# Kernel tuning notes

Measured on AMD Instinct MI355X. Metric: run time of the kernel, lower is better.

The kernel has to match this reference:

```python
import jax, jax.numpy as jnp
import numpy as np

N = 50000   # nodes
E = 600000  # edges
D = 128     # in = hidden = out channels (must be equal per the cat/mean readout)
B = 4096    # number of lookup indices


def setup_inputs() -> dict:
    key = jax.random.key(0)
    ks = jax.random.split(key, 8)
    x = jax.random.normal(ks[0], (N, D), dtype=jnp.float32)
    edge_index = jax.random.randint(ks[1], (2, E), 0, N)
    edge_weight = jax.random.uniform(ks[2], (E,), dtype=jnp.float32)
    inputs_idx = jax.random.randint(ks[3], (B,), 0, N + 1)  # N is the appended zero row
    def lin_w(k, din, dout):
        return jax.random.normal(k, (din, dout), dtype=jnp.float32) / np.sqrt(din).astype(np.float32)
    W1 = lin_w(ks[4], D, D); b1 = jnp.zeros((D,), jnp.float32)
    W2 = lin_w(ks[5], D, D); b2 = jnp.zeros((D,), jnp.float32)
    W3 = lin_w(ks[6], D, D); b3 = jnp.zeros((D,), jnp.float32)
    return {"inputs_idx": inputs_idx, "x": x, "edge_index": edge_index,
            "edge_weight": edge_weight, "W1": W1, "b1": b1, "W2": W2,
            "b2": b2, "W3": W3, "b3": b3}


def gcn_conv(x, W, b, src, dst, w):
    # PyG GCNConv with add_self_loops=True (fill weight 1) and symmetric norm.
    deg = jnp.zeros((N,), x.dtype).at[dst].add(w) + 1.0  # self-loop contributes 1
    dinv = jax.lax.rsqrt(deg)
    norm = dinv[src] * w * dinv[dst]                      # [E]
    h = x @ W                                             # [N, D]
    agg = jax.ops.segment_sum(norm[:, None] * h[src], dst, num_segments=N)
    agg = agg + h * (dinv * dinv)[:, None]                # self-loop term: deg^-1 * h
    return agg + b


def lookup(x, inputs_idx):
    # append a zero row, then gather
    x_ = jnp.concatenate([x, jnp.zeros((1, x.shape[-1]), x.dtype)], axis=0)
    return x_[inputs_idx]  # [B, D]


def reference(inputs_idx, x, edge_index, edge_weight, W1, b1, W2, b2, W3, b3):
    src, dst = edge_index[0], edge_index[1]
    x1 = jax.nn.relu(gcn_conv(x, W1, b1, src, dst, edge_weight))
    x2 = jax.nn.relu(gcn_conv(x1, W2, b2, src, dst, edge_weight))
    x3 = jax.nn.relu(gcn_conv(x2, W3, b3, src, dst, edge_weight))
    e1 = lookup(x1, inputs_idx)
    e2 = lookup(x2, inputs_idx)
    e3 = lookup(x3, inputs_idx)
    # torch.cat([1,B,D]x3, dim=0).mean(0) == elementwise mean of the three
    return (e1 + e2 + e3) / 3.0
```

## Files before the change

kernel.cpp:

```cpp
#include <hip/hip_runtime.h>
#include <hip/hip_fp16.h>

#define D 128
#define STRIDE 48

typedef _Float16 f16x8 __attribute__((ext_vector_type(8)));
typedef float f32x4 __attribute__((ext_vector_type(4)));
struct h4 { __half2 a, b; };

__global__ __launch_bounds__(256) void build_kernel(
    const int* __restrict__ ei, const float* __restrict__ ew,
    unsigned long long* __restrict__ packed, int2* __restrict__ pairs, int E) {
  int e = blockIdx.x * 256 + threadIdx.x;
  if (e >= E) return;
  int s = ei[e], d = ei[E + e];
  float w = ew[e];
  unsigned long long add =
      (1ull << 40) | (unsigned long long)(unsigned int)__float2uint_rn(w * 16777216.0f);
  unsigned long long old = atomicAdd(&packed[d], add);
  int rank = (int)(old >> 40);
  if (rank < STRIDE) pairs[(size_t)d * STRIDE + rank] = make_int2(s, __float_as_int(w));
}

__global__ __launch_bounds__(256) void dinv_cnt_kernel(
    const unsigned long long* __restrict__ packed, float* __restrict__ dinv,
    int* __restrict__ cnt, int N) {
  int i = blockIdx.x * 256 + threadIdx.x;
  if (i >= N) return;
  unsigned long long p = packed[i];
  int c = (int)(p >> 40);
  cnt[i] = c < STRIDE ? c : STRIDE;
  float deg = (float)(p & ((1ull << 40) - 1)) * (1.0f / 16777216.0f) + 1.0f;
  dinv[i] = rsqrtf(deg);
}

__global__ __launch_bounds__(256) void tohalf_kernel(
    const float* __restrict__ in, __half* __restrict__ out, int n4) {
  int t = blockIdx.x * 256 + threadIdx.x;
  if (t >= n4) return;
  float4 v = ((const float4*)in)[t];
  h4 o = {__floats2half2_rn(v.x, v.y), __floats2half2_rn(v.z, v.w)};
  ((h4*)out)[t] = o;
}

__global__ __launch_bounds__(256) void wtrans_kernel(
    const float* __restrict__ W1, const float* __restrict__ W2,
    const float* __restrict__ W3, __half* __restrict__ WT1,
    __half* __restrict__ WT2, __half* __restrict__ WT3) {
  int t = blockIdx.x * 256 + threadIdx.x;
  if (t >= 3 * D * D) return;
  int m = t >> 14;
  int i = t & (D * D - 1);
  int k = i >> 7, n = i & 127;
  const float* W = (m == 0) ? W1 : (m == 1) ? W2 : W3;
  __half* WT = (m == 0) ? WT1 : (m == 1) ? WT2 : WT3;
  WT[n * D + k] = __float2half(W[k * D + n]);
}

__global__ __launch_bounds__(256) void agg_kernel(
    const __half* __restrict__ x16, const float* __restrict__ dinv,
    const int* __restrict__ cnt, const int2* __restrict__ pairs,
    __half* __restrict__ agg16, int N) {
  int gw = (blockIdx.x * 256 + threadIdx.x) >> 6;
  int lane = threadIdx.x & 63;
  if (gw >= N) return;
  float di = dinv[gw];
  int c = cnt[gw];
  const int2* pr = pairs + (size_t)gw * STRIDE;
  float2 acc = __half22float2(((const __half2*)(x16 + (size_t)gw * D))[lane]);
  acc.x *= di * di;
  acc.y *= di * di;
  int e = 0;
  for (; e + 4 <= c; e += 4) {
    int2 p0 = pr[e], p1 = pr[e + 1], p2 = pr[e + 2], p3 = pr[e + 3];
    float n0 = dinv[p0.x] * __int_as_float(p0.y) * di;
    float n1 = dinv[p1.x] * __int_as_float(p1.y) * di;
    float n2 = dinv[p2.x] * __int_as_float(p2.y) * di;
    float n3 = dinv[p3.x] * __int_as_float(p3.y) * di;
    float2 v0 = __half22float2(((const __half2*)(x16 + (size_t)p0.x * D))[lane]);
    float2 v1 = __half22float2(((const __half2*)(x16 + (size_t)p1.x * D))[lane]);
    float2 v2 = __half22float2(((const __half2*)(x16 + (size_t)p2.x * D))[lane]);
    float2 v3 = __half22float2(((const __half2*)(x16 + (size_t)p3.x * D))[lane]);
    acc.x += n0 * v0.x + n1 * v1.x + n2 * v2.x + n3 * v3.x;
    acc.y += n0 * v0.y + n1 * v1.y + n2 * v2.y + n3 * v3.y;
  }
  for (; e < c; e++) {
    int2 p0 = pr[e];
    float n0 = dinv[p0.x] * __int_as_float(p0.y) * di;
    float2 v0 = __half22float2(((const __half2*)(x16 + (size_t)p0.x * D))[lane]);
    acc.x += n0 * v0.x;
    acc.y += n0 * v0.y;
  }
  ((__half2*)(agg16 + (size_t)gw * D))[lane] = __floats2half2_rn(acc.x, acc.y);
}

__global__ __launch_bounds__(256) void gemm16(
    const __half* __restrict__ A16, const __half* __restrict__ WT,
    const float* __restrict__ bias, __half* __restrict__ out16, int n) {
  __shared__ __half Bs[D * D];
  const int tid = threadIdx.x;
  const int wid = tid >> 6;
  const int lane = tid & 63;
  const int l15 = lane & 15;
  const int lk = lane >> 4;
  const int rbase = blockIdx.x * 64 + wid * 16;

  f16x8 a[4];
  {
    int r = rbase + l15;
    bool ok = (r < n);
    const __half* arow = A16 + (size_t)r * D + lk * 8;
#pragma unroll
    for (int kk = 0; kk < 4; kk++) {
      f16x8 z = {0, 0, 0, 0, 0, 0, 0, 0};
      a[kk] = ok ? *(const f16x8*)(arow + kk * 32) : z;
    }
  }
  {
    const int4* src = (const int4*)WT;
#pragma unroll
    for (int i = 0; i < 8; i++) {
      int slot = tid + i * 256;
      int byte = slot << 4;
      int row = byte >> 8;
      int4 v = src[slot];
      *(int4*)((char*)Bs + (byte ^ ((row & 7) << 4))) = v;
    }
  }
  __syncthreads();

  f32x4 c[8];
#pragma unroll
  for (int nf = 0; nf < 8; nf++) c[nf] = (f32x4){0.f, 0.f, 0.f, 0.f};

#pragma unroll
  for (int kk = 0; kk < 4; kk++) {
#pragma unroll
    for (int nf = 0; nf < 8; nf++) {
      int byte = ((nf * 16 + l15) << 8) + (kk << 6) + (lk << 4);
      byte ^= (l15 & 7) << 4;
      f16x8 b = *(const f16x8*)((const char*)Bs + byte);
      c[nf] = __builtin_amdgcn_mfma_f32_16x16x32_f16(a[kk], b, c[nf], 0, 0, 0);
    }
  }

#pragma unroll
  for (int nf = 0; nf < 8; nf++) {
    float bv = bias[nf * 16 + l15];
    int r0 = rbase + lk * 4;
#pragma unroll
    for (int rg = 0; rg < 4; rg++) {
      int r = r0 + rg;
      if (r < n) {
        float v = fmaxf(c[nf][rg] + bv, 0.f);
        out16[(size_t)r * D + nf * 16 + l15] = __float2half(v);
      }
    }
  }
}

__global__ __launch_bounds__(256) void lookup_kernel(
    const __half* __restrict__ xl, const int* __restrict__ idx,
    float* __restrict__ out, int B, int N, int add) {
  int t = blockIdx.x * 256 + threadIdx.x;
  if (t >= B * 16) return;
  int b = t >> 4, c8 = t & 15;
  int id = idx[b];
  float4 o0 = make_float4(0.f, 0.f, 0.f, 0.f);
  float4 o1 = make_float4(0.f, 0.f, 0.f, 0.f);
  if ((unsigned)id < (unsigned)N) {
    int4 raw = *(const int4*)(xl + (size_t)id * D + c8 * 8);
    const __half2* h = (const __half2*)&raw;
    float2 f0 = __half22float2(h[0]);
    float2 f1 = __half22float2(h[1]);
    float2 f2 = __half22float2(h[2]);
    float2 f3 = __half22float2(h[3]);
    o0 = make_float4(f0.x, f0.y, f1.x, f1.y);
    o1 = make_float4(f2.x, f2.y, f3.x, f3.y);
  }
  const float s = 1.0f / 3.0f;
  float* op = out + (size_t)b * D + c8 * 8;
  if (add) {
    float4 p0 = *(float4*)op, p1 = *(float4*)(op + 4);
    p0.x += o0.x * s; p0.y += o0.y * s; p0.z += o0.z * s; p0.w += o0.w * s;
    p1.x += o1.x * s; p1.y += o1.y * s; p1.z += o1.z * s; p1.w += o1.w * s;
    *(float4*)op = p0; *(float4*)(op + 4) = p1;
  } else {
    float4 p0 = make_float4(o0.x * s, o0.y * s, o0.z * s, o0.w * s);
    float4 p1 = make_float4(o1.x * s, o1.y * s, o1.z * s, o1.w * s);
    *(float4*)op = p0; *(float4*)(op + 4) = p1;
  }
}


extern "C" void kernel_launch(void* const* d_in, const int* in_sizes, int n_in,
                              void* d_out, int out_size, void* d_ws, size_t ws_size,
                              hipStream_t stream) {
  const int*   inputs_idx  = (const int*)d_in[0];
  const float* x           = (const float*)d_in[1];
  const int*   edge_index  = (const int*)d_in[2];
  const float* edge_weight = (const float*)d_in[3];
  const float* W1 = (const float*)d_in[4];
  const float* b1 = (const float*)d_in[5];
  const float* W2 = (const float*)d_in[6];
  const float* b2 = (const float*)d_in[7];
  const float* W3 = (const float*)d_in[8];
  const float* b3 = (const float*)d_in[9];
  float* out = (float*)d_out;

  const int B = in_sizes[0];
  const int N = in_sizes[1] / D;
  const int E = in_sizes[3];
  (void)n_in; (void)out_size; (void)ws_size;

  char* p = (char*)d_ws;
  size_t off = 0;
  auto alloc = [&](size_t bytes) -> void* {
    void* r = p + off;
    off += (bytes + 255) & ~(size_t)255;
    return r;
  };
  unsigned long long* packed = (unsigned long long*)alloc((size_t)N * 8);
  float*  dinv  = (float*)alloc((size_t)N * 4);
  int*    cnt   = (int*)alloc((size_t)N * 4);
  int2*   pairs = (int2*)alloc((size_t)N * STRIDE * 8);
  __half* x16   = (__half*)alloc((size_t)N * D * 2);
  __half* aggT  = (__half*)alloc((size_t)N * D * 2);
  __half* oA    = (__half*)alloc((size_t)N * D * 2);
  __half* oB    = (__half*)alloc((size_t)N * D * 2);
  __half* WT1   = (__half*)alloc((size_t)D * D * 2);
  __half* WT2   = (__half*)alloc((size_t)D * D * 2);
  __half* WT3   = (__half*)alloc((size_t)D * D * 2);

  hipMemsetAsync(packed, 0, (size_t)N * 8, stream);

  int eb = (E + 255) / 256;
  build_kernel<<<eb, 256, 0, stream>>>(edge_index, edge_weight, packed, pairs, E);
  dinv_cnt_kernel<<<(N + 255) / 256, 256, 0, stream>>>(packed, dinv, cnt, N);
  int n4 = N * D / 4;
  tohalf_kernel<<<(n4 + 255) / 256, 256, 0, stream>>>(x, x16, n4);
  wtrans_kernel<<<(3 * D * D + 255) / 256, 256, 0, stream>>>(W1, W2, W3, WT1, WT2, WT3);

  int ab = (N + 3) / 4;
  int gb = (N + 63) / 64;
  int lb = (B * 16 + 255) / 256;

  agg_kernel<<<ab, 256, 0, stream>>>(x16, dinv, cnt, pairs, aggT, N);
  gemm16<<<gb, 256, 0, stream>>>(aggT, WT1, b1, oA, N);
  lookup_kernel<<<lb, 256, 0, stream>>>(oA, inputs_idx, out, B, N, 0);
  agg_kernel<<<ab, 256, 0, stream>>>(oA, dinv, cnt, pairs, aggT, N);
  gemm16<<<gb, 256, 0, stream>>>(aggT, WT2, b2, oB, N);
  lookup_kernel<<<lb, 256, 0, stream>>>(oB, inputs_idx, out, B, N, 1);
  agg_kernel<<<ab, 256, 0, stream>>>(oB, dinv, cnt, pairs, aggT, N);
  gemm16<<<gb, 256, 0, stream>>>(aggT, WT3, b3, oA, N);
  lookup_kernel<<<lb, 256, 0, stream>>>(oA, inputs_idx, out, B, N, 1);
}
```

Baseline: 193.2 us.

## Precompute per-edge GCN norms once and split aggregation across channel blocks

The 64-bit packed atomic (count plus fixed-point weight) becomes a plain int count atomic. Degree is now summed from the stored pair weights by a per-node wavefront reduction, and a new norm kernel rewrites each pair's weight in place as dinv[src]*w*dinv[dst]. The three aggregation passes therefore no longer gather dinv per edge. Aggregation also moves to a 2D grid where 16 lanes per node each cover a 32-channel slice across 4 y-blocks, trading fewer wasted lanes and more parallelism for re-reading the pair list four times per node.

```diff
diff --git a/kernel.cpp b/kernel.cpp
--- a/kernel.cpp
+++ b/kernel.cpp
@@ -10,28 +10,44 @@
 
 __global__ __launch_bounds__(256) void build_kernel(
     const int* __restrict__ ei, const float* __restrict__ ew,
-    unsigned long long* __restrict__ packed, int2* __restrict__ pairs, int E) {
+    int* __restrict__ cnt, int2* __restrict__ pairs, int E) {
   int e = blockIdx.x * 256 + threadIdx.x;
   if (e >= E) return;
   int s = ei[e], d = ei[E + e];
-  float w = ew[e];
-  unsigned long long add =
-      (1ull << 40) | (unsigned long long)(unsigned int)__float2uint_rn(w * 16777216.0f);
-  unsigned long long old = atomicAdd(&packed[d], add);
-  int rank = (int)(old >> 40);
-  if (rank < STRIDE) pairs[(size_t)d * STRIDE + rank] = make_int2(s, __float_as_int(w));
-}
-
-__global__ __launch_bounds__(256) void dinv_cnt_kernel(
-    const unsigned long long* __restrict__ packed, float* __restrict__ dinv,
-    int* __restrict__ cnt, int N) {
-  int i = blockIdx.x * 256 + threadIdx.x;
-  if (i >= N) return;
-  unsigned long long p = packed[i];
-  int c = (int)(p >> 40);
-  cnt[i] = c < STRIDE ? c : STRIDE;
-  float deg = (float)(p & ((1ull << 40) - 1)) * (1.0f / 16777216.0f) + 1.0f;
-  dinv[i] = rsqrtf(deg);
+  int rank = atomicAdd(&cnt[d], 1);
+  if (rank < STRIDE) pairs[(size_t)d * STRIDE + rank] = make_int2(s, __float_as_int(ew[e]));
+}
+
+__global__ __launch_bounds__(256) void deg_dinv_kernel(
+    int* __restrict__ cnt, const int2* __restrict__ pairs,
+    float* __restrict__ dinv, int N) {
+  int n = blockIdx.x * 4 + (threadIdx.x >> 6);
+  int lane = threadIdx.x & 63;
+  if (n >= N) return;
+  int c = cnt[n];
+  c = c < STRIDE ? c : STRIDE;
+  float v = (lane < c) ? __int_as_float(pairs[(size_t)n * STRIDE + lane].y) : 0.f;
+#pragma unroll
+  for (int o = 32; o > 0; o >>= 1) v += __shfl_xor(v, o, 64);
+  if (lane == 0) {
+    dinv[n] = rsqrtf(v + 1.0f);
+    cnt[n] = c;
+  }
+}
+
+__global__ __launch_bounds__(256) void norm_kernel(
+    const int* __restrict__ cnt, const float* __restrict__ dinv,
+    int2* __restrict__ pairs, int N) {
+  int n = blockIdx.x * 4 + (threadIdx.x >> 6);
+  int lane = threadIdx.x & 63;
+  if (n >= N) return;
+  int c = cnt[n];
+  float di = dinv[n];
+  if (lane < c) {
+    int2 p = pairs[(size_t)n * STRIDE + lane];
+    p.y = __float_as_int(dinv[p.x] * __int_as_float(p.y) * di);
+    pairs[(size_t)n * STRIDE + lane] = p;
+  }
 }
 
 __global__ __launch_bounds__(256) void tohalf_kernel(
@@ -61,37 +77,34 @@
     const __half* __restrict__ x16, const float* __restrict__ dinv,
     const int* __restrict__ cnt, const int2* __restrict__ pairs,
     __half* __restrict__ agg16, int N) {
-  int gw = (blockIdx.x * 256 + threadIdx.x) >> 6;
-  int lane = threadIdx.x & 63;
-  if (gw >= N) return;
-  float di = dinv[gw];
-  int c = cnt[gw];
-  const int2* pr = pairs + (size_t)gw * STRIDE;
-  float2 acc = __half22float2(((const __half2*)(x16 + (size_t)gw * D))[lane]);
+  const int l = threadIdx.x & 15;
+  const int n = blockIdx.x * 16 + (threadIdx.x >> 4);
+  if (n >= N) return;
+  const int ch2 = blockIdx.y * 16 + l;
+  const __half2* xs = (const __half2*)x16;
+  float di = dinv[n];
+  int c = cnt[n];
+  const int2* pr = pairs + (size_t)n * STRIDE;
+  float2 acc = __half22float2(xs[(size_t)n * 64 + ch2]);
   acc.x *= di * di;
   acc.y *= di * di;
   int e = 0;
-  for (; e + 4 <= c; e += 4) {
-    int2 p0 = pr[e], p1 = pr[e + 1], p2 = pr[e + 2], p3 = pr[e + 3];
-    float n0 = dinv[p0.x] * __int_as_float(p0.y) * di;
-    float n1 = dinv[p1.x] * __int_as_float(p1.y) * di;
-    float n2 = dinv[p2.x] * __int_as_float(p2.y) * di;
-    float n3 = dinv[p3.x] * __int_as_float(p3.y) * di;
-    float2 v0 = __half22float2(((const __half2*)(x16 + (size_t)p0.x * D))[lane]);
-    float2 v1 = __half22float2(((const __half2*)(x16 + (size_t)p1.x * D))[lane]);
-    float2 v2 = __half22float2(((const __half2*)(x16 + (size_t)p2.x * D))[lane]);
-    float2 v3 = __half22float2(((const __half2*)(x16 + (size_t)p3.x * D))[lane]);
-    acc.x += n0 * v0.x + n1 * v1.x + n2 * v2.x + n3 * v3.x;
-    acc.y += n0 * v0.y + n1 * v1.y + n2 * v2.y + n3 * v3.y;
-  }
-  for (; e < c; e++) {
+  for (; e + 2 <= c; e += 2) {
+    int2 p0 = pr[e], p1 = pr[e + 1];
+    float n0 = __int_as_float(p0.y), n1 = __int_as_float(p1.y);
+    float2 v0 = __half22float2(xs[(size_t)p0.x * 64 + ch2]);
+    float2 v1 = __half22float2(xs[(size_t)p1.x * 64 + ch2]);
+    acc.x += n0 * v0.x + n1 * v1.x;
+    acc.y += n0 * v0.y + n1 * v1.y;
+  }
+  if (e < c) {
     int2 p0 = pr[e];
-    float n0 = dinv[p0.x] * __int_as_float(p0.y) * di;
-    float2 v0 = __half22float2(((const __half2*)(x16 + (size_t)p0.x * D))[lane]);
+    float n0 = __int_as_float(p0.y);
+    float2 v0 = __half22float2(xs[(size_t)p0.x * 64 + ch2]);
     acc.x += n0 * v0.x;
     acc.y += n0 * v0.y;
   }
-  ((__half2*)(agg16 + (size_t)gw * D))[lane] = __floats2half2_rn(acc.x, acc.y);
+  ((__half2*)agg16)[(size_t)n * 64 + ch2] = __floats2half2_rn(acc.x, acc.y);
 }
 
 __global__ __launch_bounds__(256) void gemm16(
@@ -220,9 +233,8 @@
     off += (bytes + 255) & ~(size_t)255;
     return r;
   };
-  unsigned long long* packed = (unsigned long long*)alloc((size_t)N * 8);
+  int*    cnt   = (int*)alloc((size_t)N * 4);
   float*  dinv  = (float*)alloc((size_t)N * 4);
-  int*    cnt   = (int*)alloc((size_t)N * 4);
   int2*   pairs = (int2*)alloc((size_t)N * STRIDE * 8);
   __half* x16   = (__half*)alloc((size_t)N * D * 2);
   __half* aggT  = (__half*)alloc((size_t)N * D * 2);
@@ -232,26 +244,29 @@
   __half* WT2   = (__half*)alloc((size_t)D * D * 2);
   __half* WT3   = (__half*)alloc((size_t)D * D * 2);
 
-  hipMemsetAsync(packed, 0, (size_t)N * 8, stream);
+  hipMemsetAsync(cnt, 0, (size_t)N * 4, stream);
 
   int eb = (E + 255) / 256;
-  build_kernel<<<eb, 256, 0, stream>>>(edge_index, edge_weight, packed, pairs, E);
-  dinv_cnt_kernel<<<(N + 255) / 256, 256, 0, stream>>>(packed, dinv, cnt, N);
+  int wb = (N + 3) / 4;
+  build_kernel<<<eb, 256, 0, stream>>>(edge_index, edge_weight, cnt, pairs, E);
+  deg_dinv_kernel<<<wb, 256, 0, stream>>>(cnt, pairs, dinv, N);
+  norm_kernel<<<wb, 256, 0, stream>>>(cnt, dinv, pairs, N);
   int n4 = N * D / 4;
   tohalf_kernel<<<(n4 + 255) / 256, 256, 0, stream>>>(x, x16, n4);
   wtrans_kernel<<<(3 * D * D + 255) / 256, 256, 0, stream>>>(W1, W2, W3, WT1, WT2, WT3);
 
-  int ab = (N + 3) / 4;
+  int agx = ((N + 15) / 16 + 7) & ~7;
+  dim3 ag(agx, 4);
   int gb = (N + 63) / 64;
   int lb = (B * 16 + 255) / 256;
 
-  agg_kernel<<<ab, 256, 0, stream>>>(x16, dinv, cnt, pairs, aggT, N);
+  agg_kernel<<<ag, 256, 0, stream>>>(x16, dinv, cnt, pairs, aggT, N);
   gemm16<<<gb, 256, 0, stream>>>(aggT, WT1, b1, oA, N);
   lookup_kernel<<<lb, 256, 0, stream>>>(oA, inputs_idx, out, B, N, 0);
-  agg_kernel<<<ab, 256, 0, stream>>>(oA, dinv, cnt, pairs, aggT, N);
+  agg_kernel<<<ag, 256, 0, stream>>>(oA, dinv, cnt, pairs, aggT, N);
   gemm16<<<gb, 256, 0, stream>>>(aggT, WT2, b2, oB, N);
   lookup_kernel<<<lb, 256, 0, stream>>>(oB, inputs_idx, out, B, N, 1);
-  agg_kernel<<<ab, 256, 0, stream>>>(oB, dinv, cnt, pairs, aggT, N);
+  agg_kernel<<<ag, 256, 0, stream>>>(oB, dinv, cnt, pairs, aggT, N);
   gemm16<<<gb, 256, 0, stream>>>(aggT, WT3, b3, oA, N);
   lookup_kernel<<<lb, 256, 0, stream>>>(oA, inputs_idx, out, B, N, 1);
 }
```

New measurement: 267.2 us. 38.3% more time.
